# Performance work log

Hardware: AMD Instinct MI355X
Metric: run time of the kernel (lower is better)

The kernel has to match this reference:

```python
import jax, jax.numpy as jnp
import numpy as np
from jax import lax

DN = ('NCHW', 'OIHW', 'NCHW')

def _edge_bank():
    # All eight fixed stencils embedded in 5x5 (3x3 kernels zero-padded to center),
    # equivalent to the original per-kernel SAME conv. Order matches torch.cat order:
    # sobel_x, sobel_y, diag1, diag2, laplacian, gradient5x5, scharr_x, scharr_y
    k3 = [
        [[-1, 0, 1], [-2, 0, 2], [-1, 0, 1]],            # sobel_x
        [[-1, -2, -1], [0, 0, 0], [1, 2, 1]],            # sobel_y
        [[0, 1, 2], [-1, 0, 1], [-2, -1, 0]],            # diag1
        [[-2, -1, 0], [-1, 0, 1], [0, 1, 2]],            # diag2
        [[0, 1, 0], [1, -4, 1], [0, 1, 0]],              # laplacian
    ]
    g5 = [[-1, -2, 0, 2, 1], [-2, -3, 0, 3, 2], [-3, -4, 0, 4, 3],
          [-2, -3, 0, 3, 2], [-1, -2, 0, 2, 1]]          # gradient5x5
    s3 = [
        [[-3, 0, 3], [-10, 0, 10], [-3, 0, 3]],          # scharr_x
        [[-3, -10, -3], [0, 0, 0], [3, 10, 3]],          # scharr_y
    ]
    ks = []
    for k in k3:
        ks.append(np.pad(np.asarray(k, np.float32), 1))
    ks.append(np.asarray(g5, np.float32))
    for k in s3:
        ks.append(np.pad(np.asarray(k, np.float32), 1))
    return jnp.asarray(np.stack(ks)[:, None, :, :])  # [8,1,5,5]

EDGE_BANK = _edge_bank()

def _conv(x, w, p):
    return lax.conv_general_dilated(x, w, (1, 1), [(p, p), (p, p)], dimension_numbers=DN)

def setup_inputs() -> dict:
    key = jax.random.key(0)
    k = jax.random.split(key, 7)
    x  = jax.random.normal(k[0], (8, 1, 512, 512), jnp.float32)
    w1 = jax.random.normal(k[1], (32, 9, 3, 3), jnp.float32) * 0.05
    b1 = jax.random.normal(k[2], (32,), jnp.float32) * 0.01
    w2 = jax.random.normal(k[3], (16, 32, 3, 3), jnp.float32) * 0.05
    b2 = jax.random.normal(k[4], (16,), jnp.float32) * 0.01
    wr = jax.random.normal(k[5], (16, 1, 1, 1), jnp.float32) * 0.05
    br = jax.random.normal(k[6], (16,), jnp.float32) * 0.01
    return {"x": x, "w1": w1, "b1": b1, "w2": w2, "b2": b2, "wr": wr, "br": br}

def reference(x, w1, b1, w2, b2, wr, br):
    grads = _conv(x, EDGE_BANK, 2)                         # [B,8,H,W] all stencils in one pass
    feats = jnp.concatenate([grads, x], axis=1)            # [B,9,H,W]
    h = jax.nn.relu(_conv(feats, w1, 1) + b1[None, :, None, None])
    fused = jax.nn.relu(_conv(h, w2, 1) + b2[None, :, None, None])
    residual = _conv(x, wr, 0) + br[None, :, None, None]
    return fused + residual
```

## Files before the change

### kernel.cpp

```cpp
#include <hip/hip_runtime.h>
#include <hip/hip_bf16.h>


typedef __attribute__((ext_vector_type(8))) short bf16x8;
typedef __attribute__((ext_vector_type(4))) float f32x4;

#define XS_S 26

#define WS_A2 5120
#define WS_SB 9728
#define WS_FLT 5120
#define WS_BYTES 25600

__device__ const float EB[9][5][5] = {
 {{0,0,0,0,0},{0,-1,0,1,0},{0,-2,0,2,0},{0,-1,0,1,0},{0,0,0,0,0}},
 {{0,0,0,0,0},{0,-1,-2,-1,0},{0,0,0,0,0},{0,1,2,1,0},{0,0,0,0,0}},
 {{0,0,0,0,0},{0,0,1,2,0},{0,-1,0,1,0},{0,-2,-1,0,0},{0,0,0,0,0}},
 {{0,0,0,0,0},{0,-2,-1,0,0},{0,-1,0,1,0},{0,0,1,2,0},{0,0,0,0,0}},
 {{0,0,0,0,0},{0,0,1,0,0},{0,1,-4,1,0},{0,0,1,0,0},{0,0,0,0,0}},
 {{-1,-2,0,2,1},{-2,-3,0,3,2},{-3,-4,0,4,3},{-2,-3,0,3,2},{-1,-2,0,2,1}},
 {{0,0,0,0,0},{0,-3,0,3,0},{0,-10,0,10,0},{0,-3,0,3,0},{0,0,0,0,0}},
 {{0,0,0,0,0},{0,-3,-10,-3,0},{0,0,0,0,0},{0,3,10,3,0},{0,0,0,0,0}},
 {{0,0,0,0,0},{0,0,0,0,0},{0,0,1,0,0},{0,0,0,0,0},{0,0,0,0,0}},
};

__device__ __forceinline__ unsigned short f2bf(float f) {
    union { float f; unsigned u; } v; v.f = f;
    unsigned u = v.u + 0x7fffu + ((v.u >> 16) & 1u);
    return (unsigned short)(u >> 16);
}

__global__ __launch_bounds__(64) void setup_frags(
    const float* __restrict__ w1, const float* __restrict__ b1,
    const float* __restrict__ w2, const float* __restrict__ b2,
    const float* __restrict__ wr, const float* __restrict__ br,
    short* __restrict__ ws)
{
    const int lane = threadIdx.x;
    const int n = lane & 15, lg = lane >> 4;
    for (int mt = 0; mt < 2; ++mt)
        for (int ks = 0; ks < 5; ++ks)
            for (int i = 0; i < 8; ++i) {
                int k = 32 * ks + 8 * lg + i;
                int g = k >> 4, ch = k & 15;
                float w = (g < 9 && ch < 9) ? w1[(mt * 16 + n) * 81 + ch * 9 + g] : 0.f;
                ws[((mt * 5 + ks) * 64 + lane) * 8 + i] = (short)f2bf(w);
            }
    for (int ks = 0; ks < 9; ++ks)
        for (int i = 0; i < 8; ++i) {
            int ic = 8 * lg + i;
            ws[WS_A2 + (ks * 64 + lane) * 8 + i] = (short)f2bf(w2[n * 288 + ic * 9 + ks]);
        }
    for (int i = 0; i < 8; ++i) {
        int k = 8 * lg + i;
        float v = (k < 25 && n < 9) ? EB[n][k / 5][k % 5] : 0.f;
        ws[WS_SB + lane * 8 + i] = (short)f2bf(v);
    }
    float* wf = (float*)ws + WS_FLT + lane * 20;
    for (int r = 0; r < 4; ++r) {
        wf[r]      = b1[lg * 4 + r];
        wf[4 + r]  = b1[16 + lg * 4 + r];
        wf[8 + r]  = b2[lg * 4 + r];
        wf[12 + r] = wr[lg * 4 + r];
        wf[16 + r] = br[lg * 4 + r];
    }
}

template<bool USE_WS>
__global__ __launch_bounds__(256, 4) void fused_edge_mfma(
    const float* __restrict__ x,  const float* __restrict__ w1, const float* __restrict__ b1,
    const float* __restrict__ w2, const float* __restrict__ b2,
    const float* __restrict__ wr, const float* __restrict__ br,
    const short* __restrict__ ws, float* __restrict__ out)
{
    __shared__ short fs2[2 * 400 * 8];
    __shared__ short hs4[4 * 324 * 8];
    __shared__ short xs[24 * XS_S];

    const int tid  = threadIdx.x;
    const int lane = tid & 63;
    const int wave = tid >> 6;
    const int n    = lane & 15;
    const int lg   = lane >> 4;
    const int bx = blockIdx.x * 16, by = blockIdx.y * 16, b = blockIdx.z;

    for (int i = tid; i < 576; i += 256) {
        int r = i / 24, c = i % 24;
        int gy = by - 4 + r, gx = bx - 4 + c;
        float v = 0.f;
        if (gy >= 0 && gy < 512 && gx >= 0 && gx < 512) v = x[(b * 512 + gy) * 512 + gx];
        __hip_bfloat16 h = __float2bfloat16(v);
        xs[r * XS_S + c] = *reinterpret_cast<short*>(&h);
    }

    bf16x8 a1[2][5], a2[9], sb;
    float b1v[2][4], b2v[4], wrv[4], brv[4];
    if (USE_WS) {
#pragma unroll
        for (int mt = 0; mt < 2; ++mt)
#pragma unroll
            for (int ks = 0; ks < 5; ++ks)
                a1[mt][ks] = *reinterpret_cast<const bf16x8*>(&ws[((mt * 5 + ks) * 64 + lane) * 8]);
#pragma unroll
        for (int ks = 0; ks < 9; ++ks)
            a2[ks] = *reinterpret_cast<const bf16x8*>(&ws[WS_A2 + (ks * 64 + lane) * 8]);
        sb = *reinterpret_cast<const bf16x8*>(&ws[WS_SB + lane * 8]);
        const float* wf = (const float*)ws + WS_FLT + lane * 20;
        f32x4 t0 = *reinterpret_cast<const f32x4*>(wf);
        f32x4 t1 = *reinterpret_cast<const f32x4*>(wf + 4);
        f32x4 t2 = *reinterpret_cast<const f32x4*>(wf + 8);
        f32x4 t3 = *reinterpret_cast<const f32x4*>(wf + 12);
        f32x4 t4 = *reinterpret_cast<const f32x4*>(wf + 16);
#pragma unroll
        for (int r = 0; r < 4; ++r) {
            b1v[0][r] = t0[r]; b1v[1][r] = t1[r];
            b2v[r] = t2[r]; wrv[r] = t3[r]; brv[r] = t4[r];
        }
    } else {
#pragma unroll
        for (int mt = 0; mt < 2; ++mt)
#pragma unroll
            for (int ks = 0; ks < 5; ++ks)
#pragma unroll
                for (int i = 0; i < 8; ++i) {
                    int k = 32 * ks + 8 * lg + i;
                    int g = k >> 4, ch = k & 15;
                    float w = (g < 9 && ch < 9) ? w1[(mt * 16 + n) * 81 + ch * 9 + g] : 0.f;
                    a1[mt][ks][i] = (short)f2bf(w);
                }
#pragma unroll
        for (int ks = 0; ks < 9; ++ks)
#pragma unroll
            for (int i = 0; i < 8; ++i)
                a2[ks][i] = (short)f2bf(w2[n * 288 + (8 * lg + i) * 9 + ks]);
#pragma unroll
        for (int i = 0; i < 8; ++i) {
            int k = 8 * lg + i;
            float v = (k < 25 && n < 9) ? EB[n][k / 5][k % 5] : 0.f;
            sb[i] = (short)f2bf(v);
        }
#pragma unroll
        for (int r = 0; r < 4; ++r) {
            b1v[0][r] = b1[lg * 4 + r]; b1v[1][r] = b1[16 + lg * 4 + r];
            b2v[r] = b2[lg * 4 + r]; wrv[r] = wr[lg * 4 + r]; brv[r] = br[lg * 4 + r];
        }
    }

    int toff[8];
#pragma unroll
    for (int i = 0; i < 8; ++i) {
        int k = 8 * lg + i;
        int t = k < 25 ? k : 24;
        toff[i] = (t / 5) * XS_S + (t % 5);
    }
    int boff[5];
#pragma unroll
    for (int ks = 0; ks < 5; ++ks) {
        int g = 2 * ks + (lg >> 1); if (g > 8) g = 8;
        int dy = g / 3, dx = g - 3 * dy;
        boff[ks] = (lg & 1) * 3200 + (dy * 20 + dx) * 8;
    }

    __syncthreads();

    for (int t = wave; t < 25; t += 4) {
        int px = t * 16 + n;
        int r = px / 20, c = px - 20 * r;
        const short* base = &xs[r * XS_S + c];
        bf16x8 bv;
#pragma unroll
        for (int i = 0; i < 8; ++i) bv[i] = base[toff[i]];
        f32x4 f = {0.f, 0.f, 0.f, 0.f};
        f = __builtin_amdgcn_mfma_f32_16x16x32_bf16(sb, bv, f, 0, 0, 0);
        int fy = by + r - 2, fx = bx + c - 2;
        float m = (fy >= 0 && fy < 512 && fx >= 0 && fx < 512) ? 1.f : 0.f;
        __hip_bfloat162 p0 = __float22bfloat162_rn(make_float2(f[0] * m, f[1] * m));
        __hip_bfloat162 p1 = __float22bfloat162_rn(make_float2(f[2] * m, f[3] * m));
        uint2 wv;
        wv.x = *reinterpret_cast<unsigned*>(&p0);
        wv.y = *reinterpret_cast<unsigned*>(&p1);
        *reinterpret_cast<uint2*>(&fs2[((lg >> 1) * 400 + px) * 8 + 4 * (lg & 1)]) = wv;
    }
    __syncthreads();

    for (int t = wave; t < 21; t += 4) {
        int p  = t * 16 + n;
        int pc = p < 323 ? p : 323;
        int r1 = pc / 18, c1 = pc - 18 * r1;
        int base = (r1 * 20 + c1) * 8;
        f32x4 acc0 = {0.f,0.f,0.f,0.f}, acc1 = {0.f,0.f,0.f,0.f};
#pragma unroll
        for (int ks = 0; ks < 5; ++ks) {
            bf16x8 bf = *reinterpret_cast<const bf16x8*>(&fs2[base + boff[ks]]);
            acc0 = __builtin_amdgcn_mfma_f32_16x16x32_bf16(a1[0][ks], bf, acc0, 0, 0, 0);
            acc1 = __builtin_amdgcn_mfma_f32_16x16x32_bf16(a1[1][ks], bf, acc1, 0, 0, 0);
        }
        if (p < 324) {
            int hy = by - 1 + r1, hx = bx - 1 + c1;
            float m = (hy >= 0 && hy < 512 && hx >= 0 && hx < 512) ? 1.f : 0.f;
            __hip_bfloat162 q0 = __float22bfloat162_rn(make_float2(
                fmaxf(acc0[0] + b1v[0][0], 0.f) * m, fmaxf(acc0[1] + b1v[0][1], 0.f) * m));
            __hip_bfloat162 q1 = __float22bfloat162_rn(make_float2(
                fmaxf(acc0[2] + b1v[0][2], 0.f) * m, fmaxf(acc0[3] + b1v[0][3], 0.f) * m));
            uint2 W0; W0.x = *reinterpret_cast<unsigned*>(&q0);
            W0.y = *reinterpret_cast<unsigned*>(&q1);
            *reinterpret_cast<uint2*>(&hs4[((lg >> 1) * 324 + p) * 8 + 4 * (lg & 1)]) = W0;
            __hip_bfloat162 q2 = __float22bfloat162_rn(make_float2(
                fmaxf(acc1[0] + b1v[1][0], 0.f) * m, fmaxf(acc1[1] + b1v[1][1], 0.f) * m));
            __hip_bfloat162 q3 = __float22bfloat162_rn(make_float2(
                fmaxf(acc1[2] + b1v[1][2], 0.f) * m, fmaxf(acc1[3] + b1v[1][3], 0.f) * m));
            uint2 W1; W1.x = *reinterpret_cast<unsigned*>(&q2);
            W1.y = *reinterpret_cast<unsigned*>(&q3);
            *reinterpret_cast<uint2*>(&hs4[((2 + (lg >> 1)) * 324 + p) * 8 + 4 * (lg & 1)]) = W1;
        }
    }
    __syncthreads();

    const int hbase = lg * 324 * 8;
#pragma unroll
    for (int j = 0; j < 4; ++j) {
        int oy = wave + 4 * j;
        f32x4 acc = {0.f,0.f,0.f,0.f};
#pragma unroll
        for (int ks = 0; ks < 9; ++ks) {
            const int dy = ks / 3, dx = ks - 3 * (ks / 3);
            bf16x8 hf = *reinterpret_cast<const bf16x8*>(
                &hs4[hbase + ((oy + dy) * 18 + n + dx) * 8]);
            acc = __builtin_amdgcn_mfma_f32_16x16x32_bf16(a2[ks], hf, acc, 0, 0, 0);
        }
        __hip_bfloat16 xh = *reinterpret_cast<const __hip_bfloat16*>(&xs[(oy + 4) * XS_S + n + 4]);
        float xv = __bfloat162float(xh);
        float* op = out + (((size_t)(b * 16 + lg * 4) * 512 + (by + oy)) * 512) + bx + n;
#pragma unroll
        for (int r = 0; r < 4; ++r) {
            float o = fmaxf(acc[r] + b2v[r], 0.f) + wrv[r] * xv + brv[r];
            __builtin_nontemporal_store(o, op);
            op += 262144;
        }
    }
}

extern "C" void kernel_launch(void* const* d_in, const int* in_sizes, int n_in,
                              void* d_out, int out_size, void* d_ws, size_t ws_size,
                              hipStream_t stream) {
    const float* x  = (const float*)d_in[0];
    const float* w1 = (const float*)d_in[1];
    const float* b1 = (const float*)d_in[2];
    const float* w2 = (const float*)d_in[3];
    const float* b2 = (const float*)d_in[4];
    const float* wr = (const float*)d_in[5];
    const float* br = (const float*)d_in[6];
    float* out = (float*)d_out;
    short* ws = (short*)d_ws;

    dim3 grid(32, 32, 8);
    dim3 block(256);
    if (ws_size >= WS_BYTES) {
        hipLaunchKernelGGL(setup_frags, dim3(1), dim3(64), 0, stream,
                           w1, b1, w2, b2, wr, br, ws);
        hipLaunchKernelGGL(fused_edge_mfma<true>, grid, block, 0, stream,
                           x, w1, b1, w2, b2, wr, br, ws, out);
    } else {
        hipLaunchKernelGGL(fused_edge_mfma<false>, grid, block, 0, stream,
                           x, w1, b1, w2, b2, wr, br, ws, out);
    }
}
```

Baseline: 95.70 us.

## Fold edge stencils into first conv weights and split interior/border kernels

Precomputes an effective 7x7 kernel per output channel by composing the fixed edge-stencil bank (plus identity) with w1. Interior tiles then compute the first layer as a direct 7x7 conv from x in two MFMAs per output pair, replacing the stencil-MFMA stage and its feature buffer in shared memory. Interior tiles use vectorized unguarded loads, less LDS and higher occupancy, while a separate border kernel keeps the original zero-padding path, where the composition is not exact. The composite weights are rounded to bf16 once, which changes rounding relative to the two-stage bf16 path.

```diff
diff --git a/kernel.cpp b/kernel.cpp
--- a/kernel.cpp
+++ b/kernel.cpp
@@ -5,12 +5,13 @@
 typedef __attribute__((ext_vector_type(8))) short bf16x8;
 typedef __attribute__((ext_vector_type(4))) float f32x4;
 
-#define XS_S 26
-
-#define WS_A2 5120
-#define WS_SB 9728
-#define WS_FLT 5120
-#define WS_BYTES 25600
+#define XS_S 28
+
+#define WS_A2   5120
+#define WS_SB   9728
+#define WS_FLT  5120
+#define WS_WEFF 12800
+#define WS_BYTES 30720
 
 __device__ const float EB[9][5][5] = {
  {{0,0,0,0,0},{0,-1,0,1,0},{0,-2,0,2,0},{0,-1,0,1,0},{0,0,0,0,0}},
@@ -28,6 +29,19 @@
     union { float f; unsigned u; } v; v.f = f;
     unsigned u = v.u + 0x7fffu + ((v.u >> 16) & 1u);
     return (unsigned short)(u >> 16);
+}
+
+__device__ __forceinline__ float weff_tap(const float* __restrict__ w1,
+                                          int oc, int dy, int dx) {
+    float s = 0.f;
+    for (int ch = 0; ch < 9; ++ch)
+        for (int ty = 0; ty < 3; ++ty)
+            for (int tx = 0; tx < 3; ++tx) {
+                int sy = dy - ty, sx = dx - tx;
+                if (sy >= 0 && sy < 5 && sx >= 0 && sx < 5)
+                    s += w1[(oc * 9 + ch) * 9 + ty * 3 + tx] * EB[ch][sy][sx];
+            }
+    return s;
 }
 
 __global__ __launch_bounds__(64) void setup_frags(
@@ -56,6 +70,13 @@
         float v = (k < 25 && n < 9) ? EB[n][k / 5][k % 5] : 0.f;
         ws[WS_SB + lane * 8 + i] = (short)f2bf(v);
     }
+    for (int mt = 0; mt < 2; ++mt)
+        for (int ks = 0; ks < 2; ++ks)
+            for (int i = 0; i < 8; ++i) {
+                int dy = 4 * ks + lg, dx = i;
+                float s = (dy < 7 && dx < 7) ? weff_tap(w1, mt * 16 + n, dy, dx) : 0.f;
+                ws[WS_WEFF + ((mt * 2 + ks) * 64 + lane) * 8 + i] = (short)f2bf(s);
+            }
     float* wf = (float*)ws + WS_FLT + lane * 20;
     for (int r = 0; r < 4; ++r) {
         wf[r]      = b1[lg * 4 + r];
@@ -67,7 +88,148 @@
 }
 
 template<bool USE_WS>
-__global__ __launch_bounds__(256, 4) void fused_edge_mfma(
+__global__ __launch_bounds__(256, 6) void edge_interior(
+    const float* __restrict__ x,  const float* __restrict__ w1, const float* __restrict__ b1,
+    const float* __restrict__ w2, const float* __restrict__ b2,
+    const float* __restrict__ wr, const float* __restrict__ br,
+    const short* __restrict__ ws, float* __restrict__ out)
+{
+    __shared__ short hs4[4 * 324 * 8];
+    __shared__ short xs[24 * XS_S];
+
+    const int tid  = threadIdx.x;
+    const int lane = tid & 63;
+    const int wave = tid >> 6;
+    const int n    = lane & 15;
+    const int lg   = lane >> 4;
+    const int bx = (blockIdx.x + 1) * 16, by = (blockIdx.y + 1) * 16, b = blockIdx.z;
+
+    if (tid < 144) {
+        int r = tid / 6, q = tid % 6;
+        const float4 v = *reinterpret_cast<const float4*>(
+            &x[((size_t)b * 512 + by - 4 + r) * 512 + bx - 4 + 4 * q]);
+        __hip_bfloat162 p0 = __float22bfloat162_rn(make_float2(v.x, v.y));
+        __hip_bfloat162 p1 = __float22bfloat162_rn(make_float2(v.z, v.w));
+        uint2 wv; wv.x = *reinterpret_cast<unsigned*>(&p0);
+        wv.y = *reinterpret_cast<unsigned*>(&p1);
+        *reinterpret_cast<uint2*>(&xs[r * XS_S + 4 * q]) = wv;
+    } else if (tid < 168) {
+        int r = tid - 144;
+        uint2 z; z.x = 0u; z.y = 0u;
+        *reinterpret_cast<uint2*>(&xs[r * XS_S + 24]) = z;
+    }
+
+    bf16x8 wa[2][2], a2[9];
+    float b1v[2][4], b2v[4], wrv[4], brv[4];
+    if (USE_WS) {
+#pragma unroll
+        for (int mt = 0; mt < 2; ++mt)
+#pragma unroll
+            for (int ks = 0; ks < 2; ++ks)
+                wa[mt][ks] = *reinterpret_cast<const bf16x8*>(
+                    &ws[WS_WEFF + ((mt * 2 + ks) * 64 + lane) * 8]);
+#pragma unroll
+        for (int ks = 0; ks < 9; ++ks)
+            a2[ks] = *reinterpret_cast<const bf16x8*>(&ws[WS_A2 + (ks * 64 + lane) * 8]);
+        const float* wf = (const float*)ws + WS_FLT + lane * 20;
+        f32x4 t0 = *reinterpret_cast<const f32x4*>(wf);
+        f32x4 t1 = *reinterpret_cast<const f32x4*>(wf + 4);
+        f32x4 t2 = *reinterpret_cast<const f32x4*>(wf + 8);
+        f32x4 t3 = *reinterpret_cast<const f32x4*>(wf + 12);
+        f32x4 t4 = *reinterpret_cast<const f32x4*>(wf + 16);
+#pragma unroll
+        for (int r = 0; r < 4; ++r) {
+            b1v[0][r] = t0[r]; b1v[1][r] = t1[r];
+            b2v[r] = t2[r]; wrv[r] = t3[r]; brv[r] = t4[r];
+        }
+    } else {
+#pragma unroll
+        for (int mt = 0; mt < 2; ++mt)
+#pragma unroll
+            for (int ks = 0; ks < 2; ++ks)
+#pragma unroll
+                for (int i = 0; i < 8; ++i) {
+                    int dy = 4 * ks + lg, dx = i;
+                    float s = (dy < 7 && dx < 7) ? weff_tap(w1, mt * 16 + n, dy, dx) : 0.f;
+                    wa[mt][ks][i] = (short)f2bf(s);
+                }
+#pragma unroll
+        for (int ks = 0; ks < 9; ++ks)
+#pragma unroll
+            for (int i = 0; i < 8; ++i)
+                a2[ks][i] = (short)f2bf(w2[n * 288 + (8 * lg + i) * 9 + ks]);
+#pragma unroll
+        for (int r = 0; r < 4; ++r) {
+            b1v[0][r] = b1[lg * 4 + r]; b1v[1][r] = b1[16 + lg * 4 + r];
+            b2v[r] = b2[lg * 4 + r]; wrv[r] = wr[lg * 4 + r]; brv[r] = br[lg * 4 + r];
+        }
+    }
+
+    __syncthreads();
+
+    for (int t = wave; t < 21; t += 4) {
+        int p  = t * 16 + n;
+        int pc = p < 323 ? p : 323;
+        int r1 = pc / 18, c1 = pc - 18 * r1;
+        int base = r1 * XS_S + c1;
+        f32x4 acc0 = {0.f,0.f,0.f,0.f}, acc1 = {0.f,0.f,0.f,0.f};
+#pragma unroll
+        for (int ks = 0; ks < 2; ++ks) {
+            const int dy = 4 * ks + lg;
+            bf16x8 bv = {0,0,0,0,0,0,0,0};
+            if (dy < 7) {
+                const short* rp = &xs[base + dy * XS_S];
+#pragma unroll
+                for (int i = 0; i < 8; ++i) bv[i] = rp[i];
+            }
+            acc0 = __builtin_amdgcn_mfma_f32_16x16x32_bf16(wa[0][ks], bv, acc0, 0, 0, 0);
+            acc1 = __builtin_amdgcn_mfma_f32_16x16x32_bf16(wa[1][ks], bv, acc1, 0, 0, 0);
+        }
+        if (p < 324) {
+            __hip_bfloat162 q0 = __float22bfloat162_rn(make_float2(
+                fmaxf(acc0[0] + b1v[0][0], 0.f), fmaxf(acc0[1] + b1v[0][1], 0.f)));
+            __hip_bfloat162 q1 = __float22bfloat162_rn(make_float2(
+                fmaxf(acc0[2] + b1v[0][2], 0.f), fmaxf(acc0[3] + b1v[0][3], 0.f)));
+            uint2 W0; W0.x = *reinterpret_cast<unsigned*>(&q0);
+            W0.y = *reinterpret_cast<unsigned*>(&q1);
+            *reinterpret_cast<uint2*>(&hs4[((lg >> 1) * 324 + p) * 8 + 4 * (lg & 1)]) = W0;
+            __hip_bfloat162 q2 = __float22bfloat162_rn(make_float2(
+                fmaxf(acc1[0] + b1v[1][0], 0.f), fmaxf(acc1[1] + b1v[1][1], 0.f)));
+            __hip_bfloat162 q3 = __float22bfloat162_rn(make_float2(
+                fmaxf(acc1[2] + b1v[1][2], 0.f), fmaxf(acc1[3] + b1v[1][3], 0.f)));
+            uint2 W1; W1.x = *reinterpret_cast<unsigned*>(&q2);
+            W1.y = *reinterpret_cast<unsigned*>(&q3);
+            *reinterpret_cast<uint2*>(&hs4[((2 + (lg >> 1)) * 324 + p) * 8 + 4 * (lg & 1)]) = W1;
+        }
+    }
+    __syncthreads();
+
+    const int hbase = lg * 324 * 8;
+#pragma unroll
+    for (int j = 0; j < 4; ++j) {
+        int oy = wave + 4 * j;
+        f32x4 acc = {0.f,0.f,0.f,0.f};
+#pragma unroll
+        for (int ks = 0; ks < 9; ++ks) {
+            const int dy = ks / 3, dx = ks - 3 * (ks / 3);
+            bf16x8 hf = *reinterpret_cast<const bf16x8*>(
+                &hs4[hbase + ((oy + dy) * 18 + n + dx) * 8]);
+            acc = __builtin_amdgcn_mfma_f32_16x16x32_bf16(a2[ks], hf, acc, 0, 0, 0);
+        }
+        __hip_bfloat16 xh = *reinterpret_cast<const __hip_bfloat16*>(&xs[(oy + 4) * XS_S + n + 4]);
+        float xv = __bfloat162float(xh);
+        float* op = out + (((size_t)(b * 16 + lg * 4) * 512 + (by + oy)) * 512) + bx + n;
+#pragma unroll
+        for (int r = 0; r < 4; ++r) {
+            float o = fmaxf(acc[r] + b2v[r], 0.f) + wrv[r] * xv + brv[r];
+            __builtin_nontemporal_store(o, op);
+            op += 262144;
+        }
+    }
+}
+
+template<bool USE_WS>
+__global__ __launch_bounds__(256, 4) void edge_border(
     const float* __restrict__ x,  const float* __restrict__ w1, const float* __restrict__ b1,
     const float* __restrict__ w2, const float* __restrict__ b2,
     const float* __restrict__ wr, const float* __restrict__ br,
@@ -82,13 +244,19 @@
     const int wave = tid >> 6;
     const int n    = lane & 15;
     const int lg   = lane >> 4;
-    const int bx = blockIdx.x * 16, by = blockIdx.y * 16, b = blockIdx.z;
+
+    int idx = blockIdx.x, tx, ty;
+    if      (idx < 32) { tx = idx;      ty = 0;  }
+    else if (idx < 64) { tx = idx - 32; ty = 31; }
+    else if (idx < 94) { tx = 0;        ty = idx - 63; }
+    else               { tx = 31;       ty = idx - 93; }
+    const int bx = tx * 16, by = ty * 16, b = blockIdx.z;
 
     for (int i = tid; i < 576; i += 256) {
         int r = i / 24, c = i % 24;
         int gy = by - 4 + r, gx = bx - 4 + c;
         float v = 0.f;
-        if (gy >= 0 && gy < 512 && gx >= 0 && gx < 512) v = x[(b * 512 + gy) * 512 + gx];
+        if (gy >= 0 && gy < 512 && gx >= 0 && gx < 512) v = x[((size_t)b * 512 + gy) * 512 + gx];
         __hip_bfloat16 h = __float2bfloat16(v);
         xs[r * XS_S + c] = *reinterpret_cast<short*>(&h);
     }
@@ -253,15 +421,20 @@
     float* out = (float*)d_out;
     short* ws = (short*)d_ws;
 
-    dim3 grid(32, 32, 8);
     dim3 block(256);
+    dim3 gin(30, 30, 8);
+    dim3 gbd(124, 1, 8);
     if (ws_size >= WS_BYTES) {
         hipLaunchKernelGGL(setup_frags, dim3(1), dim3(64), 0, stream,
                            w1, b1, w2, b2, wr, br, ws);
-        hipLaunchKernelGGL(fused_edge_mfma<true>, grid, block, 0, stream,
+        hipLaunchKernelGGL(edge_interior<true>, gin, block, 0, stream,
+                           x, w1, b1, w2, b2, wr, br, ws, out);
+        hipLaunchKernelGGL(edge_border<true>, gbd, block, 0, stream,
                            x, w1, b1, w2, b2, wr, br, ws, out);
     } else {
-        hipLaunchKernelGGL(fused_edge_mfma<false>, grid, block, 0, stream,
+        hipLaunchKernelGGL(edge_interior<false>, gin, block, 0, stream,
                            x, w1, b1, w2, b2, wr, br, ws, out);
-    }
-}
+        hipLaunchKernelGGL(edge_border<false>, gbd, block, 0, stream,
+                           x, w1, b1, w2, b2, wr, br, ws, out);
+    }
+}
```

After: 241.4 us. 152% more time.
